# Kernel tuning notes

Hardware: AMD Instinct MI355X
Metric: run time of the kernel (lower is better)

The kernel has to match this reference:

```python
import jax, jax.numpy as jnp
import numpy as np
import math

H = 16        # num query heads
KV = 4        # num key/value heads
HD = 128      # head_dim
THETA = 10000.0

def _rope(x, cos, sin):
    # x: [B, h, S, HD]; cos/sin: [1, 1, S, HD//2]
    xr, xi = x[..., :HD // 2], x[..., HD // 2:]
    return jnp.concatenate([xr * cos - xi * sin, xr * sin + xi * cos], axis=-1)

def setup_inputs() -> dict:
    key = jax.random.key(0)
    ks = jax.random.split(key, 5)
    B, S, D = 1, 4096, 2048
    s = 1.0 / math.sqrt(D)
    return {
        "hidden_states": jax.random.normal(ks[0], (B, S, D), jnp.float32),
        "Wq": jax.random.normal(ks[1], (D, H * HD), jnp.float32) * s,
        "Wk": jax.random.normal(ks[2], (D, KV * HD), jnp.float32) * s,
        "Wv": jax.random.normal(ks[3], (D, KV * HD), jnp.float32) * s,
        "Wo": jax.random.normal(ks[4], (H * HD, D), jnp.float32) * s,
    }

def reference(hidden_states, Wq, Wk, Wv, Wo):
    B, S, D = hidden_states.shape
    # projections -> [B, h, S, HD]
    q = (hidden_states @ Wq).reshape(B, S, H, HD).transpose(0, 2, 1, 3)
    k = (hidden_states @ Wk).reshape(B, S, KV, HD).transpose(0, 2, 1, 3)
    v = (hidden_states @ Wv).reshape(B, S, KV, HD).transpose(0, 2, 1, 3)
    # rotary embedding (half-split layout, matching the torch module)
    inv_freq = 1.0 / (THETA ** (jnp.arange(0, HD, 2, dtype=jnp.float32) / HD))
    freqs = jnp.arange(S, dtype=jnp.float32)[:, None] * inv_freq[None, :]  # [S, HD//2]
    cos = jnp.cos(freqs)[None, None]
    sin = jnp.sin(freqs)[None, None]
    q = _rope(q, cos, sin)
    k = _rope(k, cos, sin)
    # GQA: repeat KV heads to match query heads
    rep = H // KV
    k = jnp.repeat(k, rep, axis=1)
    v = jnp.repeat(v, rep, axis=1)
    # non-causal scaled dot-product attention (world_size==1 path)
    scores = jnp.einsum('bhqd,bhkd->bhqk', q, k) / math.sqrt(HD)
    w = jax.nn.softmax(scores, axis=-1)
    o = jnp.einsum('bhqk,bhkd->bhqd', w, v)
    o = o.transpose(0, 2, 1, 3).reshape(B, S, H * HD)
    return o @ Wo
```

## Files before the change

kernel.cpp:

```cpp
#include <hip/hip_runtime.h>
#include <math.h>

#define S_LEN 4096
#define D_MODEL 2048
#define N_HEADS 16
#define N_KV 4
#define HEAD_DIM 128
#define KV_D 512
#define QKV_N 3072
#define SM_SHIFT 18.0f

typedef short bf16x8 __attribute__((ext_vector_type(8)));
typedef float f32x4 __attribute__((ext_vector_type(4)));

#if __has_builtin(__builtin_amdgcn_exp2f)
#define EXP2(x) __builtin_amdgcn_exp2f(x)
#else
#define EXP2(x) exp2f(x)
#endif

#define SBAR() asm volatile("s_barrier" ::: "memory")
#define VMCNT(n) asm volatile("s_waitcnt vmcnt(" #n ")" ::: "memory")

static __device__ __forceinline__ float b2f(unsigned short h) {
  return __uint_as_float(((unsigned int)h) << 16);
}
static __device__ __forceinline__ unsigned int cvt_pk_bf16(float a, float b) {
  unsigned int r;
  asm("v_cvt_pk_bf16_f32 %0, %1, %2" : "=v"(r) : "v"(a), "v"(b));
  return r;
}
static __device__ __forceinline__ unsigned short f2b(float f) {
  return (unsigned short)cvt_pk_bf16(f, f);
}

static __device__ __forceinline__ void gload_lds16(const unsigned short* g,
                                                   unsigned short* l) {
  __builtin_amdgcn_global_load_lds(
      (const __attribute__((address_space(1))) void*)g,
      (__attribute__((address_space(3))) void*)l, 16, 0, 0);
}

__global__ __launch_bounds__(256) void prep_kernel(
    const float* __restrict__ X, const float* __restrict__ Wq,
    const float* __restrict__ Wk, const float* __restrict__ Wv,
    const float* __restrict__ Wo, unsigned short* __restrict__ Xb,
    unsigned short* __restrict__ Wqkv, unsigned short* __restrict__ WoT) {
  __shared__ float tile[32][33];
  const int b = blockIdx.x, t = threadIdx.x;
  if (b < 4096) {
    int i = b * 2048 + t * 8;
    float4 a = *(const float4*)(X + i);
    float4 v = *(const float4*)(X + i + 4);
    unsigned int tmp[4] = {cvt_pk_bf16(a.x, a.y), cvt_pk_bf16(a.z, a.w),
                           cvt_pk_bf16(v.x, v.y), cvt_pk_bf16(v.z, v.w)};
    *(uint4*)&Xb[i] = *(uint4*)tmp;
    return;
  }
  int id = b - 4096;
  const float* src;
  unsigned short* dst;
  int N, tc, rowOff;
  if (id < 4096) { src = Wq; dst = Wqkv; N = 2048; tc = 64; rowOff = 0; }
  else if (id < 5120) { id -= 4096; src = Wk; dst = Wqkv; N = 512; tc = 16; rowOff = 2048; }
  else if (id < 6144) { id -= 5120; src = Wv; dst = Wqkv; N = 512; tc = 16; rowOff = 2560; }
  else { id -= 6144; src = Wo; dst = WoT; N = 2048; tc = 64; rowOff = 0; }
  const int c0 = (id % tc) * 32, r0 = (id / tc) * 32;
  const int col = t & 31, rb = t >> 5;
#pragma unroll
  for (int i = 0; i < 4; i++)
    tile[rb + i * 8][col] = src[(size_t)(r0 + rb + i * 8) * N + c0 + col];
  __syncthreads();
#pragma unroll
  for (int i = 0; i < 4; i++)
    dst[(size_t)(rowOff + c0 + rb + i * 8) * 2048 + r0 + col] =
        f2b(tile[col][rb + i * 8]);
}

__global__ __launch_bounds__(256) void bgemm_kernel(
    const unsigned short* __restrict__ A, const unsigned short* __restrict__ Bt,
    void* __restrict__ C, int M, int N, int K, int bf16_out) {
  __shared__ unsigned short As[128 * 32];
  __shared__ unsigned short Bs[128 * 32];

  const int t = threadIdx.x;
  const int w = t >> 6, l = t & 63;
  const int quad = l >> 4, lx = l & 15;

  const int nwg = gridDim.x * gridDim.y;
  const int orig = blockIdx.y * gridDim.x + blockIdx.x;
  const int swz = (orig & 7) * (nwg >> 3) + (orig >> 3);
  const int bx = swz % gridDim.x, by = swz / gridDim.x;
  const int row0 = by * 128, col0 = bx * 128;
  const int wr = (w >> 1) * 64, wc = (w & 1) * 64;

  f32x4 acc[4][4];
#pragma unroll
  for (int mt = 0; mt < 4; mt++)
#pragma unroll
    for (int nt = 0; nt < 4; nt++) acc[mt][nt] = (f32x4){0.f, 0.f, 0.f, 0.f};

  for (int kt = 0; kt < K; kt += 32) {
    __syncthreads();
#pragma unroll
    for (int j = 0; j < 2; j++) {
      int ch = w * 128 + j * 64 + l;
      int r = ch >> 2, kc = (ch & 3) * 8;
      gload_lds16(A + (size_t)(row0 + r) * K + kt + kc, &As[ch * 8]);
      gload_lds16(Bt + (size_t)(col0 + r) * K + kt + kc, &Bs[ch * 8]);
    }
    __syncthreads();

    bf16x8 af[4], bfr[4];
#pragma unroll
    for (int mt = 0; mt < 4; mt++)
      af[mt] = *(const bf16x8*)&As[(wr + mt * 16 + lx) * 32 + quad * 8];
#pragma unroll
    for (int nt = 0; nt < 4; nt++)
      bfr[nt] = *(const bf16x8*)&Bs[(wc + nt * 16 + lx) * 32 + quad * 8];
#pragma unroll
    for (int mt = 0; mt < 4; mt++)
#pragma unroll
      for (int nt = 0; nt < 4; nt++)
        acc[mt][nt] = __builtin_amdgcn_mfma_f32_16x16x32_bf16(af[mt], bfr[nt],
                                                              acc[mt][nt], 0, 0, 0);
  }

  if (bf16_out) {
    unsigned short* Cp = (unsigned short*)C;
#pragma unroll
    for (int mt = 0; mt < 4; mt++)
#pragma unroll
      for (int nt = 0; nt < 4; nt++)
#pragma unroll
        for (int r = 0; r < 4; r++) {
          int row = row0 + wr + mt * 16 + quad * 4 + r;
          int col = col0 + wc + nt * 16 + lx;
          Cp[(size_t)row * N + col] = f2b(acc[mt][nt][r]);
        }
  } else {
    float* Cp = (float*)C;
#pragma unroll
    for (int mt = 0; mt < 4; mt++)
#pragma unroll
      for (int nt = 0; nt < 4; nt++)
#pragma unroll
        for (int r = 0; r < 4; r++) {
          int row = row0 + wr + mt * 16 + quad * 4 + r;
          int col = col0 + wc + nt * 16 + lx;
          Cp[(size_t)row * N + col] = acc[mt][nt][r];
        }
  }
}

__global__ __launch_bounds__(256) void ropev_kernel(
    unsigned short* __restrict__ QKV, unsigned short* __restrict__ Vt) {
  const int t = threadIdx.x;
  if (blockIdx.x < 20480) {
    int id = blockIdx.x * 256 + t;
    int d = id & 63;
    int rem = id >> 6;
    int head = rem % 20;
    int s = rem / 20;
    unsigned short* p;
    float scale;
    if (head < N_HEADS) {
      p = QKV + (size_t)s * QKV_N + head * HEAD_DIM;
      scale = 0.12753139187f;
    } else {
      p = QKV + (size_t)s * QKV_N + 2048 + (head - N_HEADS) * HEAD_DIM;
      scale = 1.0f;
    }
    float inv = exp2f(-(float)d * (13.287712379549449f / 64.0f));
    float ang = (float)s * inv;
    float sn, c;
    sincosf(ang, &sn, &c);
    float xr = b2f(p[d]), xi = b2f(p[d + 64]);
    p[d] = f2b((xr * c - xi * sn) * scale);
    p[d + 64] = f2b((xr * sn + xi * c) * scale);
    return;
  }
  __shared__ unsigned short tile[32][33];
  const unsigned short* Vb = QKV + 2560;
  int id = blockIdx.x - 20480;
  const int c0 = (id & 15) * 32;
  const int s0 = (id >> 4) * 32;
  const int col = t & 31, rbase = t >> 5;
#pragma unroll
  for (int i = 0; i < 4; i++) {
    int row = rbase + i * 8;
    tile[row][col] = Vb[(size_t)(s0 + row) * QKV_N + c0 + col];
  }
  __syncthreads();
#pragma unroll
  for (int i = 0; i < 4; i++) {
    int row = rbase + i * 8;
    Vt[(size_t)(c0 + row) * S_LEN + s0 + col] = tile[col][row];
  }
}

__global__ __launch_bounds__(256, 3) void attn_kernel(
    const unsigned short* __restrict__ Qb, const unsigned short* __restrict__ Kb,
    const unsigned short* __restrict__ Vt, unsigned short* __restrict__ Ob) {
  __shared__ unsigned short Ks[64 * 128];
  __shared__ unsigned short Vs[128 * 64];
  __shared__ unsigned short Pt[4][32 * 64];

  const int t = threadIdx.x;
  const int wave = t >> 6;
  const int lane = t & 63;
  const int quad = lane >> 4;
  const int lx = lane & 15;
  const int lx7 = lx & 7;

  const int orig = blockIdx.y * gridDim.x + blockIdx.x;
  const int swz = (orig & 7) * 64 + (orig >> 3);
  const int qt = swz & 31;
  const int h = swz >> 5;
  const int kvh = h >> 2;

  const unsigned short* Kg = Kb + kvh * HEAD_DIM;
  const unsigned short* Vg = Vt + (size_t)(kvh * HEAD_DIM) * S_LEN;

  const unsigned short* Qg =
      Qb + (size_t)(qt * 128 + wave * 32) * QKV_N + h * HEAD_DIM;
  bf16x8 qf[2][4];
#pragma unroll
  for (int qs = 0; qs < 2; qs++)
#pragma unroll
    for (int ks = 0; ks < 4; ks++)
      qf[qs][ks] = *(const bf16x8*)(Qg + (size_t)(qs * 16 + lx) * QKV_N +
                                    (quad << 3) + (ks << 5));

  f32x4 oacc[2][8];
#pragma unroll
  for (int qs = 0; qs < 2; qs++)
#pragma unroll
    for (int dt = 0; dt < 8; dt++) oacc[qs][dt] = (f32x4){0.f, 0.f, 0.f, 0.f};
  float l_st[2] = {0.f, 0.f};

  const unsigned short* kgp[4];
  const unsigned short* vgp[4];
#pragma unroll
  for (int j = 0; j < 4; j++) {
    int ch = (j * 4 + wave) * 64 + lane;
    int r = ch >> 4, c = ch & 15;
    kgp[j] = Kg + (size_t)r * QKV_N + ((c ^ (r & 7)) << 3);
    int d = ch >> 3, c2 = ch & 7;
    vgp[j] = Vg + (size_t)d * S_LEN + ((c2 ^ (d & 7)) << 3);
  }

  auto stageK = [&](int kt) {
#pragma unroll
    for (int j = 0; j < 4; j++) {
      int ch = (j * 4 + wave) * 64 + lane;
      gload_lds16(kgp[j] + (size_t)kt * (64 * QKV_N), &Ks[ch * 8]);
    }
  };
  auto stageV = [&](int kt) {
#pragma unroll
    for (int j = 0; j < 4; j++) {
      int ch = (j * 4 + wave) * 64 + lane;
      gload_lds16(vgp[j] + kt * 64, &Vs[ch * 8]);
    }
  };

  stageK(0);
  stageV(0);

  for (int kt = 0; kt < S_LEN / 64; kt++) {
    VMCNT(4);
    SBAR();

#pragma unroll
    for (int ksub = 0; ksub < 4; ksub++) {
      bf16x8 kf[4];
#pragma unroll
      for (int ks = 0; ks < 4; ks++)
        kf[ks] = *(const bf16x8*)&Ks[(ksub * 16 + lx) * 128 +
                                     (((ks * 4 + quad) ^ lx7) << 3)];
#pragma unroll
      for (int qs = 0; qs < 2; qs++) {
        f32x4 a = (f32x4){-SM_SHIFT, -SM_SHIFT, -SM_SHIFT, -SM_SHIFT};
        __builtin_amdgcn_s_setprio(1);
#pragma unroll
        for (int ks = 0; ks < 4; ks++)
          a = __builtin_amdgcn_mfma_f32_16x16x32_bf16(kf[ks], qf[qs][ks], a, 0, 0, 0);
        __builtin_amdgcn_s_setprio(0);
        float p0 = EXP2(a[0]);
        float p1 = EXP2(a[1]);
        float p2 = EXP2(a[2]);
        float p3 = EXP2(a[3]);
        l_st[qs] += (p0 + p1) + (p2 + p3);
        *(uint2*)&Pt[wave][(qs * 16 + lx) * 64 +
                           (((2 * ksub + (quad >> 1)) ^ lx7) << 3) +
                           ((quad & 1) << 2)] =
            make_uint2(cvt_pk_bf16(p0, p1), cvt_pk_bf16(p2, p3));
      }
    }

    VMCNT(0);
    SBAR();
    if (kt + 1 < S_LEN / 64) stageK(kt + 1);

#pragma unroll
    for (int st = 0; st < 2; st++) {
      const int pc = ((st * 4 + quad) ^ lx7) << 3;
      bf16x8 pb0 = *(const bf16x8*)&Pt[wave][lx * 64 + pc];
      bf16x8 pb1 = *(const bf16x8*)&Pt[wave][(16 + lx) * 64 + pc];
      __builtin_amdgcn_s_setprio(1);
#pragma unroll
      for (int dt = 0; dt < 8; dt++) {
        bf16x8 vf = *(const bf16x8*)&Vs[(dt * 16 + lx) * 64 + pc];
        oacc[0][dt] = __builtin_amdgcn_mfma_f32_16x16x32_bf16(vf, pb0, oacc[0][dt], 0, 0, 0);
        oacc[1][dt] = __builtin_amdgcn_mfma_f32_16x16x32_bf16(vf, pb1, oacc[1][dt], 0, 0, 0);
      }
      __builtin_amdgcn_s_setprio(0);
    }

    SBAR();
    if (kt + 1 < S_LEN / 64) stageV(kt + 1);
  }

#pragma unroll
  for (int qs = 0; qs < 2; qs++) {
    float l = l_st[qs];
    l += __shfl_xor(l, 16);
    l += __shfl_xor(l, 32);
    float linv = 1.0f / l;
    unsigned short* ob = Ob +
        (size_t)(qt * 128 + wave * 32 + qs * 16 + lx) * D_MODEL + h * HEAD_DIM +
        quad * 4;
#pragma unroll
    for (int dt = 0; dt < 8; dt++) {
      *(uint2*)&ob[dt * 16] = make_uint2(
          cvt_pk_bf16(oacc[qs][dt][0] * linv, oacc[qs][dt][1] * linv),
          cvt_pk_bf16(oacc[qs][dt][2] * linv, oacc[qs][dt][3] * linv));
    }
  }
}

extern "C" void kernel_launch(void* const* d_in, const int* in_sizes, int n_in,
                              void* d_out, int out_size, void* d_ws,
                              size_t ws_size, hipStream_t stream) {
  const float* X = (const float*)d_in[0];
  const float* Wq = (const float*)d_in[1];
  const float* Wk = (const float*)d_in[2];
  const float* Wv = (const float*)d_in[3];
  const float* Wo = (const float*)d_in[4];
  float* out = (float*)d_out;

  const size_t MB = 1048576;
  char* ws = (char*)d_ws;
  unsigned short* Xb    = (unsigned short*)ws;
  unsigned short* WqkvT = (unsigned short*)(ws + 16 * MB);
  unsigned short* WoT   = (unsigned short*)(ws + 28 * MB);
  unsigned short* QKV   = (unsigned short*)(ws + 36 * MB);
  unsigned short* Vtr   = (unsigned short*)(ws + 60 * MB);
  unsigned short* Ob    = (unsigned short*)(ws + 64 * MB);

  dim3 blk(256);
  prep_kernel<<<14336, blk, 0, stream>>>(X, Wq, Wk, Wv, Wo, Xb, WqkvT, WoT);
  bgemm_kernel<<<dim3(QKV_N / 128, S_LEN / 128), blk, 0, stream>>>(
      Xb, WqkvT, QKV, S_LEN, QKV_N, D_MODEL, 1);
  ropev_kernel<<<20480 + 2048, blk, 0, stream>>>(QKV, Vtr);
  attn_kernel<<<dim3(S_LEN / 128, N_HEADS), blk, 0, stream>>>(
      QKV, QKV + 2048, Vtr, Ob);
  bgemm_kernel<<<dim3(D_MODEL / 128, S_LEN / 128), blk, 0, stream>>>(
      Ob, WoT, out, S_LEN, D_MODEL, D_MODEL, 0);
}
```

Before: 380.4 us.

## Deepen GEMM K-tile with swizzled LDS and halve attention query tile per block

The GEMM now stages 64-wide K slices per iteration with an XOR-swizzled LDS layout, which halves the number of barriers per K and is meant to reduce bank conflicts. The attention kernel gives each wave 16 query rows instead of 32 and launches twice as many blocks, with launch bounds raised to 4 blocks per SM. The intent is more occupancy and better load balance across CUs. The cost is that each K/V tile staged into LDS is reused by half as many queries, so global and LDS traffic per unit of work doubles.

Measured after the change: 413.3 us. +8.6%, slower.

```diff
diff --git a/kernel.cpp b/kernel.cpp
--- a/kernel.cpp
+++ b/kernel.cpp
@@ -80,12 +80,12 @@
 __global__ __launch_bounds__(256) void bgemm_kernel(
     const unsigned short* __restrict__ A, const unsigned short* __restrict__ Bt,
     void* __restrict__ C, int M, int N, int K, int bf16_out) {
-  __shared__ unsigned short As[128 * 32];
-  __shared__ unsigned short Bs[128 * 32];
+  __shared__ unsigned short As[128 * 64];
+  __shared__ unsigned short Bs[128 * 64];
 
   const int t = threadIdx.x;
   const int w = t >> 6, l = t & 63;
-  const int quad = l >> 4, lx = l & 15;
+  const int quad = l >> 4, lx = l & 15, lx7 = lx & 7;
 
   const int nwg = gridDim.x * gridDim.y;
   const int orig = blockIdx.y * gridDim.x + blockIdx.x;
@@ -94,36 +94,50 @@
   const int row0 = by * 128, col0 = bx * 128;
   const int wr = (w >> 1) * 64, wc = (w & 1) * 64;
 
+  const unsigned short* agp[4];
+  const unsigned short* bgp[4];
+#pragma unroll
+  for (int j = 0; j < 4; j++) {
+    int ch = j * 256 + t;
+    int r = ch >> 3, c = ch & 7;
+    agp[j] = A + (size_t)(row0 + r) * K + ((c ^ (r & 7)) << 3);
+    bgp[j] = Bt + (size_t)(col0 + r) * K + ((c ^ (r & 7)) << 3);
+  }
+
   f32x4 acc[4][4];
 #pragma unroll
   for (int mt = 0; mt < 4; mt++)
 #pragma unroll
     for (int nt = 0; nt < 4; nt++) acc[mt][nt] = (f32x4){0.f, 0.f, 0.f, 0.f};
 
-  for (int kt = 0; kt < K; kt += 32) {
+  for (int kt = 0; kt < K; kt += 64) {
     __syncthreads();
 #pragma unroll
-    for (int j = 0; j < 2; j++) {
-      int ch = w * 128 + j * 64 + l;
-      int r = ch >> 2, kc = (ch & 3) * 8;
-      gload_lds16(A + (size_t)(row0 + r) * K + kt + kc, &As[ch * 8]);
-      gload_lds16(Bt + (size_t)(col0 + r) * K + kt + kc, &Bs[ch * 8]);
+    for (int j = 0; j < 4; j++) {
+      int ch = j * 256 + t;
+      gload_lds16(agp[j] + kt, &As[ch * 8]);
+      gload_lds16(bgp[j] + kt, &Bs[ch * 8]);
     }
     __syncthreads();
 
-    bf16x8 af[4], bfr[4];
-#pragma unroll
-    for (int mt = 0; mt < 4; mt++)
-      af[mt] = *(const bf16x8*)&As[(wr + mt * 16 + lx) * 32 + quad * 8];
-#pragma unroll
-    for (int nt = 0; nt < 4; nt++)
-      bfr[nt] = *(const bf16x8*)&Bs[(wc + nt * 16 + lx) * 32 + quad * 8];
-#pragma unroll
-    for (int mt = 0; mt < 4; mt++)
+#pragma unroll
+    for (int kk = 0; kk < 2; kk++) {
+      bf16x8 af[4], bfr[4];
+#pragma unroll
+      for (int mt = 0; mt < 4; mt++)
+        af[mt] = *(const bf16x8*)&As[(wr + mt * 16 + lx) * 64 +
+                                     (((kk * 4 + quad) ^ lx7) << 3)];
 #pragma unroll
       for (int nt = 0; nt < 4; nt++)
-        acc[mt][nt] = __builtin_amdgcn_mfma_f32_16x16x32_bf16(af[mt], bfr[nt],
-                                                              acc[mt][nt], 0, 0, 0);
+        bfr[nt] = *(const bf16x8*)&Bs[(wc + nt * 16 + lx) * 64 +
+                                      (((kk * 4 + quad) ^ lx7) << 3)];
+#pragma unroll
+      for (int mt = 0; mt < 4; mt++)
+#pragma unroll
+        for (int nt = 0; nt < 4; nt++)
+          acc[mt][nt] = __builtin_amdgcn_mfma_f32_16x16x32_bf16(
+              af[mt], bfr[nt], acc[mt][nt], 0, 0, 0);
+    }
   }
 
   if (bf16_out) {
@@ -199,12 +213,12 @@
   }
 }
 
-__global__ __launch_bounds__(256, 3) void attn_kernel(
+__global__ __launch_bounds__(256, 4) void attn_kernel(
     const unsigned short* __restrict__ Qb, const unsigned short* __restrict__ Kb,
     const unsigned short* __restrict__ Vt, unsigned short* __restrict__ Ob) {
   __shared__ unsigned short Ks[64 * 128];
   __shared__ unsigned short Vs[128 * 64];
-  __shared__ unsigned short Pt[4][32 * 64];
+  __shared__ unsigned short Pt[4][16 * 64];
 
   const int t = threadIdx.x;
   const int wave = t >> 6;
@@ -214,30 +228,25 @@
   const int lx7 = lx & 7;
 
   const int orig = blockIdx.y * gridDim.x + blockIdx.x;
-  const int swz = (orig & 7) * 64 + (orig >> 3);
-  const int qt = swz & 31;
-  const int h = swz >> 5;
+  const int swz = (orig & 7) * 128 + (orig >> 3);
+  const int qt = swz & 63;
+  const int h = swz >> 6;
   const int kvh = h >> 2;
 
   const unsigned short* Kg = Kb + kvh * HEAD_DIM;
   const unsigned short* Vg = Vt + (size_t)(kvh * HEAD_DIM) * S_LEN;
 
   const unsigned short* Qg =
-      Qb + (size_t)(qt * 128 + wave * 32) * QKV_N + h * HEAD_DIM;
-  bf16x8 qf[2][4];
-#pragma unroll
-  for (int qs = 0; qs < 2; qs++)
-#pragma unroll
-    for (int ks = 0; ks < 4; ks++)
-      qf[qs][ks] = *(const bf16x8*)(Qg + (size_t)(qs * 16 + lx) * QKV_N +
-                                    (quad << 3) + (ks << 5));
-
-  f32x4 oacc[2][8];
-#pragma unroll
-  for (int qs = 0; qs < 2; qs++)
-#pragma unroll
-    for (int dt = 0; dt < 8; dt++) oacc[qs][dt] = (f32x4){0.f, 0.f, 0.f, 0.f};
-  float l_st[2] = {0.f, 0.f};
+      Qb + (size_t)(qt * 64 + wave * 16) * QKV_N + h * HEAD_DIM;
+  bf16x8 qf[4];
+#pragma unroll
+  for (int ks = 0; ks < 4; ks++)
+    qf[ks] = *(const bf16x8*)(Qg + (size_t)lx * QKV_N + (quad << 3) + (ks << 5));
+
+  f32x4 oacc[8];
+#pragma unroll
+  for (int dt = 0; dt < 8; dt++) oacc[dt] = (f32x4){0.f, 0.f, 0.f, 0.f};
+  float l_st = 0.f;
 
   const unsigned short* kgp[4];
   const unsigned short* vgp[4];
@@ -279,24 +288,20 @@
       for (int ks = 0; ks < 4; ks++)
         kf[ks] = *(const bf16x8*)&Ks[(ksub * 16 + lx) * 128 +
                                      (((ks * 4 + quad) ^ lx7) << 3)];
-#pragma unroll
-      for (int qs = 0; qs < 2; qs++) {
-        f32x4 a = (f32x4){-SM_SHIFT, -SM_SHIFT, -SM_SHIFT, -SM_SHIFT};
-        __builtin_amdgcn_s_setprio(1);
-#pragma unroll
-        for (int ks = 0; ks < 4; ks++)
-          a = __builtin_amdgcn_mfma_f32_16x16x32_bf16(kf[ks], qf[qs][ks], a, 0, 0, 0);
-        __builtin_amdgcn_s_setprio(0);
-        float p0 = EXP2(a[0]);
-        float p1 = EXP2(a[1]);
-        float p2 = EXP2(a[2]);
-        float p3 = EXP2(a[3]);
-        l_st[qs] += (p0 + p1) + (p2 + p3);
-        *(uint2*)&Pt[wave][(qs * 16 + lx) * 64 +
-                           (((2 * ksub + (quad >> 1)) ^ lx7) << 3) +
-                           ((quad & 1) << 2)] =
-            make_uint2(cvt_pk_bf16(p0, p1), cvt_pk_bf16(p2, p3));
-      }
+      f32x4 a = (f32x4){-SM_SHIFT, -SM_SHIFT, -SM_SHIFT, -SM_SHIFT};
+      __builtin_amdgcn_s_setprio(1);
+#pragma unroll
+      for (int ks = 0; ks < 4; ks++)
+        a = __builtin_amdgcn_mfma_f32_16x16x32_bf16(kf[ks], qf[ks], a, 0, 0, 0);
+      __builtin_amdgcn_s_setprio(0);
+      float p0 = EXP2(a[0]);
+      float p1 = EXP2(a[1]);
+      float p2 = EXP2(a[2]);
+      float p3 = EXP2(a[3]);
+      l_st += (p0 + p1) + (p2 + p3);
+      *(uint2*)&Pt[wave][lx * 64 + (((2 * ksub + (quad >> 1)) ^ lx7) << 3) +
+                         ((quad & 1) << 2)] =
+          make_uint2(cvt_pk_bf16(p0, p1), cvt_pk_bf16(p2, p3));
     }
 
     VMCNT(0);
@@ -306,14 +311,12 @@
 #pragma unroll
     for (int st = 0; st < 2; st++) {
       const int pc = ((st * 4 + quad) ^ lx7) << 3;
-      bf16x8 pb0 = *(const bf16x8*)&Pt[wave][lx * 64 + pc];
-      bf16x8 pb1 = *(const bf16x8*)&Pt[wave][(16 + lx) * 64 + pc];
+      bf16x8 pb = *(const bf16x8*)&Pt[wave][lx * 64 + pc];
       __builtin_amdgcn_s_setprio(1);
 #pragma unroll
       for (int dt = 0; dt < 8; dt++) {
         bf16x8 vf = *(const bf16x8*)&Vs[(dt * 16 + lx) * 64 + pc];
-        oacc[0][dt] = __builtin_amdgcn_mfma_f32_16x16x32_bf16(vf, pb0, oacc[0][dt], 0, 0, 0);
-        oacc[1][dt] = __builtin_amdgcn_mfma_f32_16x16x32_bf16(vf, pb1, oacc[1][dt], 0, 0, 0);
+        oacc[dt] = __builtin_amdgcn_mfma_f32_16x16x32_bf16(vf, pb, oacc[dt], 0, 0, 0);
       }
       __builtin_amdgcn_s_setprio(0);
     }
@@ -322,20 +325,18 @@
     if (kt + 1 < S_LEN / 64) stageV(kt + 1);
   }
 
-#pragma unroll
-  for (int qs = 0; qs < 2; qs++) {
-    float l = l_st[qs];
+  {
+    float l = l_st;
     l += __shfl_xor(l, 16);
     l += __shfl_xor(l, 32);
     float linv = 1.0f / l;
     unsigned short* ob = Ob +
-        (size_t)(qt * 128 + wave * 32 + qs * 16 + lx) * D_MODEL + h * HEAD_DIM +
-        quad * 4;
+        (size_t)(qt * 64 + wave * 16 + lx) * D_MODEL + h * HEAD_DIM + quad * 4;
 #pragma unroll
     for (int dt = 0; dt < 8; dt++) {
       *(uint2*)&ob[dt * 16] = make_uint2(
-          cvt_pk_bf16(oacc[qs][dt][0] * linv, oacc[qs][dt][1] * linv),
-          cvt_pk_bf16(oacc[qs][dt][2] * linv, oacc[qs][dt][3] * linv));
+          cvt_pk_bf16(oacc[dt][0] * linv, oacc[dt][1] * linv),
+          cvt_pk_bf16(oacc[dt][2] * linv, oacc[dt][3] * linv));
     }
   }
 }
@@ -364,7 +365,7 @@
   bgemm_kernel<<<dim3(QKV_N / 128, S_LEN / 128), blk, 0, stream>>>(
       Xb, WqkvT, QKV, S_LEN, QKV_N, D_MODEL, 1);
   ropev_kernel<<<20480 + 2048, blk, 0, stream>>>(QKV, Vtr);
-  attn_kernel<<<dim3(S_LEN / 128, N_HEADS), blk, 0, stream>>>(
+  attn_kernel<<<dim3(S_LEN / 64, N_HEADS), blk, 0, stream>>>(
       QKV, QKV + 2048, Vtr, Ob);
   bgemm_kernel<<<dim3(D_MODEL / 128, S_LEN / 128), blk, 0, stream>>>(
       Ob, WoT, out, S_LEN, D_MODEL, D_MODEL, 0);
```
